# Optimization experiments

Measured on AMD Instinct MI355X. Metric: run time of the kernel, lower is better.

Reference implementation:

```python
import jax, jax.numpy as jnp
import numpy as np

EPS = 0.001  # variance floor from the original module


def setup_inputs() -> dict:
    key = jax.random.key(0)
    k1, k2, k3, k4, k5, k6 = jax.random.split(key, 6)
    N = 2_000_000  # total anchors
    V = 500_000    # valid (sampled) anchors
    bbox_pred = jax.random.normal(k1, (1, N, 4), dtype=jnp.float32)
    bbox_uncertainty_pred = jax.random.normal(k2, (1, N, 4), dtype=jnp.float32)
    bbox_class = jax.random.normal(k3, (1, N, 2), dtype=jnp.float32)
    gt_bbox = jax.random.normal(k4, (1, N, 4), dtype=jnp.float32)
    gt_anchor_label = jax.random.randint(k5, (1, N), 0, 2, dtype=jnp.int32)
    valid_indices = jnp.sort(jax.random.randint(k6, (1, V), 0, N, dtype=jnp.int32), axis=-1)
    return {
        "bbox_pred": bbox_pred,
        "bbox_uncertainty_pred": bbox_uncertainty_pred,
        "bbox_class": bbox_class,
        "gt_bbox": gt_bbox,
        "gt_anchor_label": gt_anchor_label,
        "valid_indices": valid_indices,
    }


def reference(bbox_pred, bbox_uncertainty_pred, bbox_class, gt_bbox,
              gt_anchor_label, valid_indices):
    vi = valid_indices[0]                       # [V]
    labels = gt_anchor_label[0][vi]             # [V]

    # ---- classification: CrossEntropyLoss (mean over valid anchors) ----
    logits = bbox_class[0][vi]                  # [V, 2]
    logp = jax.nn.log_softmax(logits, axis=-1)
    class_loss = -jnp.mean(jnp.take_along_axis(logp, labels[:, None].astype(jnp.int32), axis=-1))

    pred = bbox_pred[0][vi]                     # [V, 4]
    unc = bbox_uncertainty_pred[0][vi]          # [V, 4]
    gt = gt_bbox[0][vi]                         # [V, 4]
    var = EPS + unc * unc                       # [V, 4]

    pos_term = (0.5 * (pred - gt) ** 2 / var + 0.5 * jnp.log(var)).sum(axis=-1)  # [V]
    neg_term = (1.0 / var).sum(axis=-1)                                          # [V]

    pos = (labels == 1).astype(jnp.float32)     # [V]
    n_pos = pos.sum()
    n_neg = (1.0 - pos).sum()
    reg_loss = (pos_term * pos).sum() / n_pos + (neg_term * (1.0 - pos)).sum() / n_neg

    return class_loss + reg_loss
```

## Files before the change

### kernel.cpp

```cpp
#include <hip/hip_runtime.h>

#define EPS_VAR 0.001f

__device__ __forceinline__ double wave_reduce(double v) {
    #pragma unroll
    for (int off = 32; off > 0; off >>= 1)
        v += __shfl_down(v, off, 64);
    return v;
}

__global__ __launch_bounds__(256) void rpn_pass1(
    const float* __restrict__ pred,
    const float* __restrict__ unc,
    const float* __restrict__ cls,
    const float* __restrict__ gt,
    const int* __restrict__ lab,
    const int* __restrict__ vi,
    int V,
    double* __restrict__ out_part) {

    double s_cls = 0.0, s_pos = 0.0, s_neg = 0.0;
    int n_pos = 0, n_neg = 0;

    const int stride = gridDim.x * blockDim.x;
    for (int i = blockIdx.x * blockDim.x + threadIdx.x; i < V; i += stride) {
        const int idx = vi[i];
        const int l = lab[idx];

        const float2 lg = *reinterpret_cast<const float2*>(cls + 2ll * idx);
        const float m = fmaxf(lg.x, lg.y);
        const float lse = m + logf(expf(lg.x - m) + expf(lg.y - m));
        s_cls += (double)(lse - ((l == 1) ? lg.y : lg.x));

        const float4 u = *reinterpret_cast<const float4*>(unc + 4ll * idx);
        const float v0 = EPS_VAR + u.x * u.x;
        const float v1 = EPS_VAR + u.y * u.y;
        const float v2 = EPS_VAR + u.z * u.z;
        const float v3 = EPS_VAR + u.w * u.w;

        if (l == 1) {
            const float4 p = *reinterpret_cast<const float4*>(pred + 4ll * idx);
            const float4 g = *reinterpret_cast<const float4*>(gt + 4ll * idx);
            const float d0 = p.x - g.x, d1 = p.y - g.y;
            const float d2 = p.z - g.z, d3 = p.w - g.w;
            const float t = 0.5f * (d0 * d0 / v0 + d1 * d1 / v1 +
                                    d2 * d2 / v2 + d3 * d3 / v3)
                          + 0.5f * (logf(v0) + logf(v1) + logf(v2) + logf(v3));
            s_pos += (double)t;
            n_pos++;
        } else {
            const float t = 1.0f / v0 + 1.0f / v1 + 1.0f / v2 + 1.0f / v3;
            s_neg += (double)t;
            n_neg++;
        }
    }

    __shared__ double sh[4][5];
    const double r0 = wave_reduce(s_cls);
    const double r1 = wave_reduce(s_pos);
    const double r2 = wave_reduce(s_neg);
    const double r3 = wave_reduce((double)n_pos);
    const double r4 = wave_reduce((double)n_neg);

    const int wave = threadIdx.x >> 6;
    if ((threadIdx.x & 63) == 0) {
        sh[wave][0] = r0; sh[wave][1] = r1; sh[wave][2] = r2;
        sh[wave][3] = r3; sh[wave][4] = r4;
    }
    __syncthreads();
    if (threadIdx.x == 0) {
        double a0 = 0, a1 = 0, a2 = 0, a3 = 0, a4 = 0;
        #pragma unroll
        for (int w = 0; w < 4; ++w) {
            a0 += sh[w][0]; a1 += sh[w][1]; a2 += sh[w][2];
            a3 += sh[w][3]; a4 += sh[w][4];
        }
        double* o = out_part + 5ll * blockIdx.x;
        o[0] = a0; o[1] = a1; o[2] = a2; o[3] = a3; o[4] = a4;
    }
}

__global__ __launch_bounds__(256) void rpn_pass2(
    const double* __restrict__ part, int nb, int V, float* __restrict__ out) {

    double a0 = 0, a1 = 0, a2 = 0, a3 = 0, a4 = 0;
    for (int i = threadIdx.x; i < nb; i += blockDim.x) {
        const double* p = part + 5ll * i;
        a0 += p[0]; a1 += p[1]; a2 += p[2]; a3 += p[3]; a4 += p[4];
    }

    __shared__ double sh[4][5];
    a0 = wave_reduce(a0);
    a1 = wave_reduce(a1);
    a2 = wave_reduce(a2);
    a3 = wave_reduce(a3);
    a4 = wave_reduce(a4);

    const int wave = threadIdx.x >> 6;
    if ((threadIdx.x & 63) == 0) {
        sh[wave][0] = a0; sh[wave][1] = a1; sh[wave][2] = a2;
        sh[wave][3] = a3; sh[wave][4] = a4;
    }
    __syncthreads();
    if (threadIdx.x == 0) {
        double t0 = 0, t1 = 0, t2 = 0, t3 = 0, t4 = 0;
        #pragma unroll
        for (int w = 0; w < 4; ++w) {
            t0 += sh[w][0]; t1 += sh[w][1]; t2 += sh[w][2];
            t3 += sh[w][3]; t4 += sh[w][4];
        }
        const double class_loss = t0 / (double)V;
        const double reg_loss = t1 / t3 + t2 / t4;
        out[0] = (float)(class_loss + reg_loss);
    }
}

extern "C" void kernel_launch(void* const* d_in, const int* in_sizes, int n_in,
                              void* d_out, int out_size, void* d_ws, size_t ws_size,
                              hipStream_t stream) {
    const float* pred = (const float*)d_in[0];
    const float* unc  = (const float*)d_in[1];
    const float* cls  = (const float*)d_in[2];
    const float* gt   = (const float*)d_in[3];
    const int*   lab  = (const int*)d_in[4];
    const int*   vi   = (const int*)d_in[5];
    const int V = in_sizes[5];

    const int NB = 1024;
    double* part = (double*)d_ws;

    rpn_pass1<<<NB, 256, 0, stream>>>(pred, unc, cls, gt, lab, vi, V, part);
    rpn_pass2<<<1, 256, 0, stream>>>(part, NB, V, (float*)d_out);
}
```

Baseline: 24.35 us.

## Fuse two-pass reduction into one kernel with last-block ticket finalize

Merges the partial-sum kernel and the final reduction kernel into one launch. The last block to finish, found through an atomic ticket counter, performs the final sum. The grid now covers the input exactly with two elements per thread, using int2 index loads and all gathers issued up front to raise memory-level parallelism. It also switches to fast __logf/__expf intrinsics and one log of the product of variances. This adds a memset launch for the ticket and slightly lowers numerical precision.

```diff
diff --git a/kernel.cpp b/kernel.cpp
--- a/kernel.cpp
+++ b/kernel.cpp
@@ -9,58 +9,118 @@
     return v;
 }
 
-__global__ __launch_bounds__(256) void rpn_pass1(
+__global__ __launch_bounds__(256) void rpn_fused(
     const float* __restrict__ pred,
     const float* __restrict__ unc,
     const float* __restrict__ cls,
     const float* __restrict__ gt,
     const int* __restrict__ lab,
     const int* __restrict__ vi,
-    int V,
-    double* __restrict__ out_part) {
+    int V, int NB,
+    double* __restrict__ part,
+    unsigned int* __restrict__ ticket,
+    float* __restrict__ out) {
 
     double s_cls = 0.0, s_pos = 0.0, s_neg = 0.0;
     int n_pos = 0, n_neg = 0;
 
-    const int stride = gridDim.x * blockDim.x;
-    for (int i = blockIdx.x * blockDim.x + threadIdx.x; i < V; i += stride) {
-        const int idx = vi[i];
-        const int l = lab[idx];
+    const int base = blockIdx.x * 512 + threadIdx.x * 2;
 
-        const float2 lg = *reinterpret_cast<const float2*>(cls + 2ll * idx);
-        const float m = fmaxf(lg.x, lg.y);
-        const float lse = m + logf(expf(lg.x - m) + expf(lg.y - m));
-        s_cls += (double)(lse - ((l == 1) ? lg.y : lg.x));
+    if (base + 1 < V) {
+        const int2 ii = *reinterpret_cast<const int2*>(vi + base);
+        const int idx0 = ii.x, idx1 = ii.y;
 
-        const float4 u = *reinterpret_cast<const float4*>(unc + 4ll * idx);
-        const float v0 = EPS_VAR + u.x * u.x;
-        const float v1 = EPS_VAR + u.y * u.y;
-        const float v2 = EPS_VAR + u.z * u.z;
-        const float v3 = EPS_VAR + u.w * u.w;
+        const float2 lg0 = *reinterpret_cast<const float2*>(cls + 2ll * idx0);
+        const float2 lg1 = *reinterpret_cast<const float2*>(cls + 2ll * idx1);
+        const float4 u0  = *reinterpret_cast<const float4*>(unc + 4ll * idx0);
+        const float4 u1  = *reinterpret_cast<const float4*>(unc + 4ll * idx1);
+        const int l0 = lab[idx0];
+        const int l1 = lab[idx1];
 
-        if (l == 1) {
-            const float4 p = *reinterpret_cast<const float4*>(pred + 4ll * idx);
-            const float4 g = *reinterpret_cast<const float4*>(gt + 4ll * idx);
-            const float d0 = p.x - g.x, d1 = p.y - g.y;
-            const float d2 = p.z - g.z, d3 = p.w - g.w;
-            const float t = 0.5f * (d0 * d0 / v0 + d1 * d1 / v1 +
-                                    d2 * d2 / v2 + d3 * d3 / v3)
-                          + 0.5f * (logf(v0) + logf(v1) + logf(v2) + logf(v3));
-            s_pos += (double)t;
-            n_pos++;
-        } else {
-            const float t = 1.0f / v0 + 1.0f / v1 + 1.0f / v2 + 1.0f / v3;
-            s_neg += (double)t;
-            n_neg++;
+        {
+            const float mx = fmaxf(lg0.x, lg0.y);
+            const float dd = fabsf(lg0.x - lg0.y);
+            const float lse = mx + __logf(1.0f + __expf(-dd));
+            s_cls += (double)(lse - ((l0 == 1) ? lg0.y : lg0.x));
+
+            const float v0 = EPS_VAR + u0.x * u0.x;
+            const float v1 = EPS_VAR + u0.y * u0.y;
+            const float v2 = EPS_VAR + u0.z * u0.z;
+            const float v3 = EPS_VAR + u0.w * u0.w;
+            if (l0 == 1) {
+                const float4 p = *reinterpret_cast<const float4*>(pred + 4ll * idx0);
+                const float4 g = *reinterpret_cast<const float4*>(gt + 4ll * idx0);
+                const float d0 = p.x - g.x, d1 = p.y - g.y;
+                const float d2 = p.z - g.z, d3 = p.w - g.w;
+                s_pos += (double)(0.5f * (d0 * d0 / v0 + d1 * d1 / v1 +
+                                          d2 * d2 / v2 + d3 * d3 / v3)
+                                  + 0.5f * __logf(v0 * v1 * v2 * v3));
+                n_pos++;
+            } else {
+                s_neg += (double)(1.0f / v0 + 1.0f / v1 + 1.0f / v2 + 1.0f / v3);
+                n_neg++;
+            }
+        }
+        {
+            const float mx = fmaxf(lg1.x, lg1.y);
+            const float dd = fabsf(lg1.x - lg1.y);
+            const float lse = mx + __logf(1.0f + __expf(-dd));
+            s_cls += (double)(lse - ((l1 == 1) ? lg1.y : lg1.x));
+
+            const float v0 = EPS_VAR + u1.x * u1.x;
+            const float v1 = EPS_VAR + u1.y * u1.y;
+            const float v2 = EPS_VAR + u1.z * u1.z;
+            const float v3 = EPS_VAR + u1.w * u1.w;
+            if (l1 == 1) {
+                const float4 p = *reinterpret_cast<const float4*>(pred + 4ll * idx1);
+                const float4 g = *reinterpret_cast<const float4*>(gt + 4ll * idx1);
+                const float d0 = p.x - g.x, d1 = p.y - g.y;
+                const float d2 = p.z - g.z, d3 = p.w - g.w;
+                s_pos += (double)(0.5f * (d0 * d0 / v0 + d1 * d1 / v1 +
+                                          d2 * d2 / v2 + d3 * d3 / v3)
+                                  + 0.5f * __logf(v0 * v1 * v2 * v3));
+                n_pos++;
+            } else {
+                s_neg += (double)(1.0f / v0 + 1.0f / v1 + 1.0f / v2 + 1.0f / v3);
+                n_neg++;
+            }
+        }
+    } else {
+        for (int i = base; i < V && i < base + 2; ++i) {
+            const int idx = vi[i];
+            const float2 lg = *reinterpret_cast<const float2*>(cls + 2ll * idx);
+            const float4 u  = *reinterpret_cast<const float4*>(unc + 4ll * idx);
+            const int l = lab[idx];
+            const float mx = fmaxf(lg.x, lg.y);
+            const float dd = fabsf(lg.x - lg.y);
+            const float lse = mx + __logf(1.0f + __expf(-dd));
+            s_cls += (double)(lse - ((l == 1) ? lg.y : lg.x));
+            const float v0 = EPS_VAR + u.x * u.x;
+            const float v1 = EPS_VAR + u.y * u.y;
+            const float v2 = EPS_VAR + u.z * u.z;
+            const float v3 = EPS_VAR + u.w * u.w;
+            if (l == 1) {
+                const float4 p = *reinterpret_cast<const float4*>(pred + 4ll * idx);
+                const float4 g = *reinterpret_cast<const float4*>(gt + 4ll * idx);
+                const float d0 = p.x - g.x, d1 = p.y - g.y;
+                const float d2 = p.z - g.z, d3 = p.w - g.w;
+                s_pos += (double)(0.5f * (d0 * d0 / v0 + d1 * d1 / v1 +
+                                          d2 * d2 / v2 + d3 * d3 / v3)
+                                  + 0.5f * __logf(v0 * v1 * v2 * v3));
+                n_pos++;
+            } else {
+                s_neg += (double)(1.0f / v0 + 1.0f / v1 + 1.0f / v2 + 1.0f / v3);
+                n_neg++;
+            }
         }
     }
 
     __shared__ double sh[4][5];
-    const double r0 = wave_reduce(s_cls);
-    const double r1 = wave_reduce(s_pos);
-    const double r2 = wave_reduce(s_neg);
-    const double r3 = wave_reduce((double)n_pos);
-    const double r4 = wave_reduce((double)n_neg);
+    double r0 = wave_reduce(s_cls);
+    double r1 = wave_reduce(s_pos);
+    double r2 = wave_reduce(s_neg);
+    double r3 = wave_reduce((double)n_pos);
+    double r4 = wave_reduce((double)n_neg);
 
     const int wave = threadIdx.x >> 6;
     if ((threadIdx.x & 63) == 0) {
@@ -68,6 +128,8 @@
         sh[wave][3] = r3; sh[wave][4] = r4;
     }
     __syncthreads();
+
+    __shared__ int sh_last;
     if (threadIdx.x == 0) {
         double a0 = 0, a1 = 0, a2 = 0, a3 = 0, a4 = 0;
         #pragma unroll
@@ -75,43 +137,43 @@
             a0 += sh[w][0]; a1 += sh[w][1]; a2 += sh[w][2];
             a3 += sh[w][3]; a4 += sh[w][4];
         }
-        double* o = out_part + 5ll * blockIdx.x;
+        double* o = part + 5ll * blockIdx.x;
         o[0] = a0; o[1] = a1; o[2] = a2; o[3] = a3; o[4] = a4;
-    }
-}
-
-__global__ __launch_bounds__(256) void rpn_pass2(
-    const double* __restrict__ part, int nb, int V, float* __restrict__ out) {
-
-    double a0 = 0, a1 = 0, a2 = 0, a3 = 0, a4 = 0;
-    for (int i = threadIdx.x; i < nb; i += blockDim.x) {
-        const double* p = part + 5ll * i;
-        a0 += p[0]; a1 += p[1]; a2 += p[2]; a3 += p[3]; a4 += p[4];
-    }
-
-    __shared__ double sh[4][5];
-    a0 = wave_reduce(a0);
-    a1 = wave_reduce(a1);
-    a2 = wave_reduce(a2);
-    a3 = wave_reduce(a3);
-    a4 = wave_reduce(a4);
-
-    const int wave = threadIdx.x >> 6;
-    if ((threadIdx.x & 63) == 0) {
-        sh[wave][0] = a0; sh[wave][1] = a1; sh[wave][2] = a2;
-        sh[wave][3] = a3; sh[wave][4] = a4;
+        __threadfence();
+        const unsigned int t = atomicAdd(ticket, 1u);
+        sh_last = (t == (unsigned int)(NB - 1)) ? 1 : 0;
     }
     __syncthreads();
-    if (threadIdx.x == 0) {
-        double t0 = 0, t1 = 0, t2 = 0, t3 = 0, t4 = 0;
-        #pragma unroll
-        for (int w = 0; w < 4; ++w) {
-            t0 += sh[w][0]; t1 += sh[w][1]; t2 += sh[w][2];
-            t3 += sh[w][3]; t4 += sh[w][4];
+
+    if (sh_last) {
+        __threadfence();
+        double a0 = 0, a1 = 0, a2 = 0, a3 = 0, a4 = 0;
+        for (int i = threadIdx.x; i < NB; i += 256) {
+            const double* p = part + 5ll * i;
+            a0 += p[0]; a1 += p[1]; a2 += p[2]; a3 += p[3]; a4 += p[4];
         }
-        const double class_loss = t0 / (double)V;
-        const double reg_loss = t1 / t3 + t2 / t4;
-        out[0] = (float)(class_loss + reg_loss);
+        a0 = wave_reduce(a0);
+        a1 = wave_reduce(a1);
+        a2 = wave_reduce(a2);
+        a3 = wave_reduce(a3);
+        a4 = wave_reduce(a4);
+        __syncthreads();
+        if ((threadIdx.x & 63) == 0) {
+            sh[wave][0] = a0; sh[wave][1] = a1; sh[wave][2] = a2;
+            sh[wave][3] = a3; sh[wave][4] = a4;
+        }
+        __syncthreads();
+        if (threadIdx.x == 0) {
+            double t0 = 0, t1 = 0, t2 = 0, t3 = 0, t4 = 0;
+            #pragma unroll
+            for (int w = 0; w < 4; ++w) {
+                t0 += sh[w][0]; t1 += sh[w][1]; t2 += sh[w][2];
+                t3 += sh[w][3]; t4 += sh[w][4];
+            }
+            const double class_loss = t0 / (double)V;
+            const double reg_loss = t1 / t3 + t2 / t4;
+            out[0] = (float)(class_loss + reg_loss);
+        }
     }
 }
 
@@ -126,9 +188,12 @@
     const int*   vi   = (const int*)d_in[5];
     const int V = in_sizes[5];
 
-    const int NB = 1024;
-    double* part = (double*)d_ws;
+    const int NB = (V + 511) / 512;
 
-    rpn_pass1<<<NB, 256, 0, stream>>>(pred, unc, cls, gt, lab, vi, V, part);
-    rpn_pass2<<<1, 256, 0, stream>>>(part, NB, V, (float*)d_out);
+    unsigned int* ticket = (unsigned int*)d_ws;
+    double* part = (double*)((char*)d_ws + 64);
+
+    hipMemsetAsync(ticket, 0, sizeof(unsigned int), stream);
+    rpn_fused<<<NB, 256, 0, stream>>>(pred, unc, cls, gt, lab, vi, V, NB,
+                                      part, ticket, (float*)d_out);
 }
```

After: 55.74 us. 2.29x slower.
